# Optimization experiments

Measured on AMD Instinct MI355X. Metric: run time of the kernel, lower is better.

The kernel has to match this reference:

```python
import jax, jax.numpy as jnp
import numpy as np

DIM = 256
NEG_SLOPE = 0.01  # torch F.leaky_relu default


def setup_inputs() -> dict:
    key = jax.random.key(0)
    ks = jax.random.split(key, 10)
    B, O, I, D = 16, 64, 512, DIM
    q = jax.random.normal(ks[0], (B, O, D), dtype=jnp.float32)
    k = jax.random.normal(ks[1], (B, I, D), dtype=jnp.float32)
    v = jax.random.normal(ks[2], (B, I, D), dtype=jnp.float32)
    mask = jax.random.randint(ks[3], (B, I), 0, 2).astype(bool)  # 1/True = pad
    s = 1.0 / np.sqrt(2 * D)
    # score MLP: Linear(2D -> D), tanh, Linear(D -> 1)
    W1 = jax.random.normal(ks[4], (D, 2 * D), dtype=jnp.float32) * s
    b1 = jnp.zeros((D,), dtype=jnp.float32)
    W2 = jax.random.normal(ks[5], (1, D), dtype=jnp.float32) * (1.0 / np.sqrt(D))
    b2 = jnp.zeros((1,), dtype=jnp.float32)
    # output projection fw: Linear(D -> D)
    Wf = jax.random.normal(ks[6], (D, D), dtype=jnp.float32) * (1.0 / np.sqrt(D))
    bf = jnp.zeros((D,), dtype=jnp.float32)
    return {"q": q, "k": k, "v": v, "mask": mask,
            "W1": W1, "b1": b1, "W2": W2, "b2": b2, "Wf": Wf, "bf": bf}


def reference(q, k, v, mask, W1, b1, W2, b2, Wf, bf):
    # Linear over concat([q, k]) decomposes exactly: W1 @ [q;k] = W1q@q + W1k@k
    D = q.shape[-1]
    W1q, W1k = W1[:, :D], W1[:, D:]
    qp = jnp.einsum('bod,hd->boh', q, W1q)          # (B, O, D)
    kp = jnp.einsum('bid,hd->bih', k, W1k)          # (B, I, D)
    h = jnp.tanh(qp[:, :, None, :] + kp[:, None, :, :] + b1)  # (B, O, I, D)
    score = jnp.einsum('boih,h->boi', h, W2[0]) + b2[0]       # (B, O, I)
    score = jnp.where(mask[:, None, :], -jnp.inf, score)
    attn = jax.nn.softmax(score, axis=-1)           # (B, O, I)
    out = jnp.einsum('boi,bid->bod', attn, v)       # (B, O, D)
    out = out @ Wf.T + bf                           # dropout in eval mode = identity
    out = jnp.where(out >= 0, out, NEG_SLOPE * out) # leaky_relu
    return out, attn
```

## Files before the change

### kernel.cpp

```cpp
#include <hip/hip_runtime.h>
#include <math.h>

#define DIM 256
#define BATCH 16
#define NO 64
#define NI 512
#define NEG_SLOPE 0.01f
#define CSCALE 2.885390081777927f
#define OT 2

typedef float f32x4 __attribute__((ext_vector_type(4)));
typedef __bf16 bf16x8 __attribute__((ext_vector_type(8)));
typedef unsigned int u32x4 __attribute__((ext_vector_type(4)));

__device__ __forceinline__ void split2(float f, unsigned int& hi16, float& lo) {
  unsigned int u = __builtin_bit_cast(unsigned int, f);
  unsigned int h = (u + 0x7FFFu + ((u >> 16) & 1u)) & 0xFFFF0000u;
  hi16 = h >> 16;
  lo = f - __builtin_bit_cast(float, h);
}
__device__ __forceinline__ unsigned int rne16(float f) {
  unsigned int u = __builtin_bit_cast(unsigned int, f);
  return (u + 0x7FFFu + ((u >> 16) & 1u)) >> 16;
}

struct __align__(8) U2 { unsigned int x, y; };

#define OFF_AH 0
#define OFF_AL 9216
#define OFF_WH 18432
#define OFF_WL 27648

__global__ __launch_bounds__(256, 4) void proj_kernel(
    const float* __restrict__ q, const float* __restrict__ k,
    const float* __restrict__ W1, const float* __restrict__ b1,
    const float* __restrict__ Wf, const int* __restrict__ mask,
    float* __restrict__ Eq, float* __restrict__ Ek4, float* __restrict__ WfT)
{
  __shared__ __align__(16) char smemRaw[36864];
  __shared__ int idx_s[64];
  __shared__ int swtot[4];

  const int t  = threadIdx.x;
  const int bx = blockIdx.x;

  if (bx >= 576) {
    float* smem = (float*)smemRaw;
    const int tt = bx - 576;
    const int tr = tt >> 2, tc = tt & 3;
#pragma unroll
    for (int p = 0; p < 4; ++p) {
      int idx2 = p * 256 + t;
      int row = idx2 >> 4, j = idx2 & 15;
      float4 vv = *(const float4*)(Wf + (size_t)(tr * 64 + row) * 256 + tc * 64 + j * 4);
      *(float4*)&smem[row * 68 + j * 4] = vv;
    }
    __syncthreads();
#pragma unroll
    for (int p = 0; p < 4; ++p) {
      int idx2 = p * 256 + t;
      int row = idx2 >> 4, j = idx2 & 15;
      float4 ov;
      ov.x = smem[(j * 4 + 0) * 68 + row];
      ov.y = smem[(j * 4 + 1) * 68 + row];
      ov.z = smem[(j * 4 + 2) * 68 + row];
      ov.w = smem[(j * 4 + 3) * 68 + row];
      *(float4*)(WfT + (size_t)(tc * 64 + row) * 256 + tr * 64 + j * 4) = ov;
    }
    return;
  }

  const int mt = bx >> 2;
  const int nt = bx & 3;
  const int h0 = nt * 64;
  const bool isq = (mt < 16);

  const int srow = t >> 4;
  const int sc4  = t & 15;
  const int lane = t & 63, w = t >> 6;
  const int m0w = (w >> 1) * 32, n0w = (w & 1) * 32;
  const int lr = lane & 15, lg = lane >> 4;

  const float* src;
  int coff, bb = 0, jb0 = 0, cntb = 0;
  int rowg[4];

  if (isq) {
    src  = q + (size_t)(mt * 64) * DIM;
    coff = 0;
#pragma unroll
    for (int p = 0; p < 4; ++p) rowg[p] = srow + p * 16;
  } else {
    const int ki = mt - 16;
    bb  = ki >> 3;
    jb0 = (ki & 7) * 64;
    const int e0 = (mask[bb * NI + 2 * t] == 0);
    const int e1 = (mask[bb * NI + 2 * t + 1] == 0);
    const int ps = e0 + e1;
    int x = ps;
#pragma unroll
    for (int off = 1; off < 64; off <<= 1) {
      int y = __shfl_up(x, off, 64);
      if (lane >= off) x += y;
    }
    if (lane == 63) swtot[w] = x;
    if (t < 64) idx_s[t] = 0;
    __syncthreads();
    int woffv = 0;
#pragma unroll
    for (int w2 = 0; w2 < 4; ++w2) {
      int v_ = swtot[w2];
      if (w2 < w) woffv += v_;
      cntb += v_;
    }
    const int excl = woffv + x - ps;
    const int p0 = excl, p1 = excl + e0;
    if (e0 && p0 >= jb0 && p0 < jb0 + 64) idx_s[p0 - jb0] = 2 * t;
    if (e1 && p1 >= jb0 && p1 < jb0 + 64) idx_s[p1 - jb0] = 2 * t + 1;
    __syncthreads();
    if (jb0 >= cntb) return;
    src  = k + (size_t)bb * NI * DIM;
    coff = DIM;
#pragma unroll
    for (int p = 0; p < 4; ++p) rowg[p] = idx_s[srow + p * 16];
  }

  f32x4 acc[2][2] = {};

  float4 aR[4], wR[4];
#define LOADC(c0_)                                                              \
  _Pragma("unroll")                                                             \
  for (int p = 0; p < 4; ++p) {                                                 \
    aR[p] = *(const float4*)(src + (size_t)rowg[p] * DIM + (c0_) + sc4 * 4);    \
    wR[p] = *(const float4*)(W1 + (size_t)(h0 + srow + p * 16) * (2 * DIM) + coff + (c0_) + sc4 * 4); \
  }

  LOADC(0)

  for (int c = 0; c < 4; ++c) {
#pragma unroll
    for (int p = 0; p < 4; ++p) {
      int row = srow + p * 16;
      int boff = row * 144 + sc4 * 8;
      unsigned int h0_, h1_, h2_, h3_;
      float l0, l1, l2, l3;
      split2(aR[p].x, h0_, l0); split2(aR[p].y, h1_, l1);
      split2(aR[p].z, h2_, l2); split2(aR[p].w, h3_, l3);
      *(U2*)(smemRaw + OFF_AH + boff) = { h0_ | (h1_ << 16), h2_ | (h3_ << 16) };
      *(U2*)(smemRaw + OFF_AL + boff) = { rne16(l0) | (rne16(l1) << 16),
                                          rne16(l2) | (rne16(l3) << 16) };
      split2(wR[p].x, h0_, l0); split2(wR[p].y, h1_, l1);
      split2(wR[p].z, h2_, l2); split2(wR[p].w, h3_, l3);
      *(U2*)(smemRaw + OFF_WH + boff) = { h0_ | (h1_ << 16), h2_ | (h3_ << 16) };
      *(U2*)(smemRaw + OFF_WL + boff) = { rne16(l0) | (rne16(l1) << 16),
                                          rne16(l2) | (rne16(l3) << 16) };
    }
    __syncthreads();

    if (c < 3) { LOADC((c + 1) * 64) }

#pragma unroll
    for (int kk = 0; kk < 2; ++kk) {
      const int kb = kk * 64 + lg * 16;
      bf16x8 ah[2], al[2], bh[2], bl[2];
#pragma unroll
      for (int mi = 0; mi < 2; ++mi) {
        int row = m0w + mi * 16 + lr;
        ah[mi] = __builtin_bit_cast(bf16x8, *(const u32x4*)(smemRaw + OFF_AH + row * 144 + kb));
        al[mi] = __builtin_bit_cast(bf16x8, *(const u32x4*)(smemRaw + OFF_AL + row * 144 + kb));
      }
#pragma unroll
      for (int ni = 0; ni < 2; ++ni) {
        int row = n0w + ni * 16 + lr;
        bh[ni] = __builtin_bit_cast(bf16x8, *(const u32x4*)(smemRaw + OFF_WH + row * 144 + kb));
        bl[ni] = __builtin_bit_cast(bf16x8, *(const u32x4*)(smemRaw + OFF_WL + row * 144 + kb));
      }
#pragma unroll
      for (int mi = 0; mi < 2; ++mi)
#pragma unroll
        for (int ni = 0; ni < 2; ++ni) {
          acc[mi][ni] = __builtin_amdgcn_mfma_f32_16x16x32_bf16(ah[mi], bh[ni], acc[mi][ni], 0, 0, 0);
          acc[mi][ni] = __builtin_amdgcn_mfma_f32_16x16x32_bf16(ah[mi], bl[ni], acc[mi][ni], 0, 0, 0);
          acc[mi][ni] = __builtin_amdgcn_mfma_f32_16x16x32_bf16(al[mi], bh[ni], acc[mi][ni], 0, 0, 0);
        }
    }
    __syncthreads();
  }

  if (isq) {
    const int r0 = mt * 64;
#pragma unroll
    for (int ni = 0; ni < 2; ++ni) {
      int h = h0 + n0w + ni * 16 + lr;
      float b1v = b1[h];
#pragma unroll
      for (int mi = 0; mi < 2; ++mi)
#pragma unroll
        for (int rg = 0; rg < 4; ++rg) {
          int r = r0 + m0w + mi * 16 + lg * 4 + rg;
          Eq[(size_t)r * DIM + h] =
              __builtin_amdgcn_exp2f((acc[mi][ni][rg] + b1v) * CSCALE);
        }
    }
  } else {
    const int lim = cntb - jb0;
#pragma unroll
    for (int mi = 0; mi < 2; ++mi)
#pragma unroll
      for (int rg = 0; rg < 4; ++rg) {
        int local = m0w + mi * 16 + lg * 4 + rg;
        if (local < lim) {
          int pos = jb0 + local;
#pragma unroll
          for (int ni = 0; ni < 2; ++ni) {
            int h = h0 + n0w + ni * 16 + lr;
            Ek4[((size_t)(bb * 64 + (h >> 2)) * NI + pos) * 4 + (h & 3)] =
                __builtin_amdgcn_exp2f(acc[mi][ni][rg] * CSCALE);
          }
        }
      }
  }
}

__device__ __forceinline__ void f4arr(float4 v, float* a) {
  a[0] = v.x; a[1] = v.y; a[2] = v.z; a[3] = v.w;
}

__global__ __launch_bounds__(512, 4) void attn_kernel(
    const float* __restrict__ Eq, const float* __restrict__ Ek4,
    const float* __restrict__ v, const int* __restrict__ mask,
    const float* __restrict__ W2, const float* __restrict__ b2,
    const float* __restrict__ WfT, const float* __restrict__ bf,
    float* __restrict__ out, float* __restrict__ attn_out)
{
  __shared__ float sc[OT][NI];
  __shared__ int   idxs[NI];
  __shared__ float pvp[8][OT][DIM];
  __shared__ float o0[OT][DIM];
  __shared__ float red4[8][OT];
  __shared__ float redw[8];
  __shared__ int   swtot8[8];

  const int t    = threadIdx.x;
  const int lane = t & 63;
  const int wid  = t >> 6;

  const int blk  = blockIdx.x;
  const int tile = (blk & 7) * 64 + (blk >> 3);
  const int b    = tile >> 5;
  const int bo0  = b * 64 + (tile & 31) * OT;

  const int unm = (mask[b * NI + t] == 0) ? 1 : 0;
  unsigned long long bal = __ballot(unm);
  int my = __popcll(bal & ((1ull << lane) - 1ull));
  if (lane == 0) swtot8[wid] = __popcll(bal);

  float partial = (t < DIM) ? W2[t] : 0.f;
#pragma unroll
  for (int off = 32; off >= 1; off >>= 1) partial += __shfl_xor(partial, off, 64);
  if (lane == 0) redw[wid] = partial;
  __syncthreads();

  int cntb = 0, woffv = 0;
#pragma unroll
  for (int w = 0; w < 8; ++w) {
    int v_ = swtot8[w];
    if (w < wid) woffv += v_;
    cntb += v_;
  }
  const int myPos = unm ? (woffv + my) : -1;
  if (unm) idxs[myPos] = t;

  float sumw2 = 0.f;
#pragma unroll
  for (int w = 0; w < 8; ++w) sumw2 += redw[w];
  const float base = sumw2 + b2[0];

  const int j = t;
  const bool active = (j < cntb);
  const int jc = active ? j : (cntb > 0 ? cntb - 1 : 0);
  const float4* kb4 = (const float4*)Ek4 + (size_t)b * 64 * NI;
  const float* qrow0 = Eq + (size_t)(bo0 + 0) * DIM;
  const float* qrow1 = Eq + (size_t)(bo0 + 1) * DIM;

  float acc0 = 0.f, acc1 = 0.f;
  if (wid * 64 < cntb) {
#pragma unroll 8
    for (int hq = 0; hq < 64; ++hq) {
      float4 kq = kb4[(size_t)hq * NI + jc];
      float wr[4], q0r[4], q1r[4], kv[4];
      f4arr(*(const float4*)(W2 + hq * 4), wr);
      f4arr(*(const float4*)(qrow0 + hq * 4), q0r);
      f4arr(*(const float4*)(qrow1 + hq * 4), q1r);
      f4arr(kq, kv);
#pragma unroll
      for (int pr = 0; pr < 2; ++pr) {
        const int ea = pr * 2, eb = pr * 2 + 1;
        float A0 = fmaf(q0r[ea], kv[ea], 1.f);
        float B0 = fmaf(q0r[eb], kv[eb], 1.f);
        float N0 = fmaf(wr[eb], A0, wr[ea] * B0);
        acc0 = fmaf(N0, __builtin_amdgcn_rcpf(A0 * B0), acc0);
        float A1 = fmaf(q1r[ea], kv[ea], 1.f);
        float B1 = fmaf(q1r[eb], kv[eb], 1.f);
        float N1 = fmaf(wr[eb], A1, wr[ea] * B1);
        acc1 = fmaf(N1, __builtin_amdgcn_rcpf(A1 * B1), acc1);
      }
    }
  }

  float s0 = active ? (base - 2.f * acc0) : -INFINITY;
  float s1 = active ? (base - 2.f * acc1) : -INFINITY;

  float p0 = __builtin_amdgcn_exp2f(s0 * 1.4426950408889634f);
  float p1 = __builtin_amdgcn_exp2f(s1 * 1.4426950408889634f);
  float ps0 = p0, ps1 = p1;
#pragma unroll
  for (int off = 32; off >= 1; off >>= 1) {
    ps0 += __shfl_xor(ps0, off, 64);
    ps1 += __shfl_xor(ps1, off, 64);
  }
  __syncthreads();
  if (lane == 0) { red4[wid][0] = ps0; red4[wid][1] = ps1; }
  __syncthreads();
  float ss0 = 0.f, ss1 = 0.f;
#pragma unroll
  for (int w = 0; w < 8; ++w) { ss0 += red4[w][0]; ss1 += red4[w][1]; }
  const float a0 = p0 * __builtin_amdgcn_rcpf(ss0);
  const float a1 = p1 * __builtin_amdgcn_rcpf(ss1);
  sc[0][j] = a0;
  sc[1][j] = a1;
  __syncthreads();

  {
    float w0 = (myPos >= 0) ? sc[0][myPos] : 0.f;
    float w1 = (myPos >= 0) ? sc[1][myPos] : 0.f;
    attn_out[(size_t)(bo0 + 0) * NI + t] = w0;
    attn_out[(size_t)(bo0 + 1) * NI + t] = w1;
  }

  {
    const int d4 = lane;
    float4 av0 = {0.f, 0.f, 0.f, 0.f};
    float4 av1 = {0.f, 0.f, 0.f, 0.f};
    const float4* vb4 = (const float4*)(v + (size_t)b * NI * DIM);
    const int jend = min(wid * 64 + 64, cntb);
#pragma unroll 4
    for (int jb = wid * 64; jb < jend; ++jb) {
      int row = idxs[jb];
      float sa0 = sc[0][jb], sa1 = sc[1][jb];
      float4 vv = vb4[(size_t)row * 64 + d4];
      av0.x = fmaf(sa0, vv.x, av0.x);
      av0.y = fmaf(sa0, vv.y, av0.y);
      av0.z = fmaf(sa0, vv.z, av0.z);
      av0.w = fmaf(sa0, vv.w, av0.w);
      av1.x = fmaf(sa1, vv.x, av1.x);
      av1.y = fmaf(sa1, vv.y, av1.y);
      av1.z = fmaf(sa1, vv.z, av1.z);
      av1.w = fmaf(sa1, vv.w, av1.w);
    }
    *(float4*)&pvp[wid][0][d4 * 4] = av0;
    *(float4*)&pvp[wid][1][d4 * 4] = av1;
  }
  __syncthreads();
  {
    int oo = t >> 8, d = t & 255;
    float sacc = 0.f;
#pragma unroll
    for (int w = 0; w < 8; ++w) sacc += pvp[w][oo][d];
    o0[oo][d] = sacc;
  }
  __syncthreads();

  if (t < DIM) {
    const int d = t;
    float f0 = 0.f, f1 = 0.f;
#pragma unroll 8
    for (int e4 = 0; e4 < 64; ++e4) {
      float oa[4], ob[4];
      f4arr(*(const float4*)&o0[0][e4 * 4], oa);
      f4arr(*(const float4*)&o0[1][e4 * 4], ob);
#pragma unroll
      for (int c = 0; c < 4; ++c) {
        float wv = WfT[(size_t)(e4 * 4 + c) * DIM + d];
        f0 = fmaf(oa[c], wv, f0);
        f1 = fmaf(ob[c], wv, f1);
      }
    }
    float bfv = bf[d];
    f0 += bfv; f1 += bfv;
    f0 = (f0 >= 0.f) ? f0 : NEG_SLOPE * f0;
    f1 = (f1 >= 0.f) ? f1 : NEG_SLOPE * f1;
    out[(size_t)(bo0 + 0) * DIM + d] = f0;
    out[(size_t)(bo0 + 1) * DIM + d] = f1;
  }
}

extern "C" void kernel_launch(void* const* d_in, const int* in_sizes, int n_in,
                              void* d_out, int out_size, void* d_ws, size_t ws_size,
                              hipStream_t stream) {
  const float* q    = (const float*)d_in[0];
  const float* k    = (const float*)d_in[1];
  const float* v    = (const float*)d_in[2];
  const int*   mask = (const int*)d_in[3];
  const float* W1   = (const float*)d_in[4];
  const float* b1   = (const float*)d_in[5];
  const float* W2   = (const float*)d_in[6];
  const float* b2   = (const float*)d_in[7];
  const float* Wf   = (const float*)d_in[8];
  const float* bf   = (const float*)d_in[9];

  float* out      = (float*)d_out;
  float* attn_out = out + (size_t)BATCH * NO * DIM;

  float* Eq   = (float*)d_ws;
  float* Ek4  = Eq + (size_t)BATCH * NO * DIM;
  float* WfT  = Ek4 + (size_t)BATCH * DIM * NI;

  proj_kernel<<<592, 256, 0, stream>>>(q, k, W1, b1, Wf, mask, Eq, Ek4, WfT);
  attn_kernel<<<(BATCH * NO) / OT, 512, 0, stream>>>(Eq, Ek4, v, mask,
                                                     W2, b2, WfT, bf, out, attn_out);
}
```

Measured before the change: 121.6 us.

## Process four query rows per attention block and stage q rows in LDS

Raises the number of output rows per block from two to four, so each Ek4 and v load is reused across more queries. The block count halves and the tile mapping is adjusted to match. The query rows are now staged in shared memory instead of being read from global memory inside the hot loop. In exchange, register and LDS use per block grow, so launch bounds drop to 2 blocks per CU, and with fewer blocks occupancy and latency hiding may suffer.

```diff
diff --git a/kernel.cpp b/kernel.cpp
--- a/kernel.cpp
+++ b/kernel.cpp
@@ -7,7 +7,7 @@
 #define NI 512
 #define NEG_SLOPE 0.01f
 #define CSCALE 2.885390081777927f
-#define OT 2
+#define OT 4
 
 typedef float f32x4 __attribute__((ext_vector_type(4)));
 typedef __bf16 bf16x8 __attribute__((ext_vector_type(8)));
@@ -226,7 +226,7 @@
   a[0] = v.x; a[1] = v.y; a[2] = v.z; a[3] = v.w;
 }
 
-__global__ __launch_bounds__(512, 4) void attn_kernel(
+__global__ __launch_bounds__(512, 2) void attn_kernel(
     const float* __restrict__ Eq, const float* __restrict__ Ek4,
     const float* __restrict__ v, const int* __restrict__ mask,
     const float* __restrict__ W2, const float* __restrict__ b2,
@@ -235,6 +235,7 @@
 {
   __shared__ float sc[OT][NI];
   __shared__ int   idxs[NI];
+  __shared__ float qs[OT][DIM];
   __shared__ float pvp[8][OT][DIM];
   __shared__ float o0[OT][DIM];
   __shared__ float red4[8][OT];
@@ -246,15 +247,21 @@
   const int wid  = t >> 6;
 
   const int blk  = blockIdx.x;
-  const int tile = (blk & 7) * 64 + (blk >> 3);
-  const int b    = tile >> 5;
-  const int bo0  = b * 64 + (tile & 31) * OT;
+  const int tile = (blk & 7) * 32 + (blk >> 3);
+  const int b    = tile >> 4;
+  const int bo0  = b * 64 + (tile & 15) * OT;
 
   const int unm = (mask[b * NI + t] == 0) ? 1 : 0;
   unsigned long long bal = __ballot(unm);
   int my = __popcll(bal & ((1ull << lane) - 1ull));
   if (lane == 0) swtot8[wid] = __popcll(bal);
 
+  if (t < 256) {
+    const int r = t >> 6, part = t & 63;
+    *(float4*)&qs[r][part * 4] =
+        *(const float4*)(Eq + (size_t)(bo0 + r) * DIM + part * 4);
+  }
+
   float partial = (t < DIM) ? W2[t] : 0.f;
 #pragma unroll
   for (int off = 32; off >= 1; off >>= 1) partial += __shfl_xor(partial, off, 64);
@@ -280,118 +287,124 @@
   const bool active = (j < cntb);
   const int jc = active ? j : (cntb > 0 ? cntb - 1 : 0);
   const float4* kb4 = (const float4*)Ek4 + (size_t)b * 64 * NI;
-  const float* qrow0 = Eq + (size_t)(bo0 + 0) * DIM;
-  const float* qrow1 = Eq + (size_t)(bo0 + 1) * DIM;
-
-  float acc0 = 0.f, acc1 = 0.f;
+
+  float accv[OT] = {};
   if (wid * 64 < cntb) {
-#pragma unroll 8
+#pragma unroll 4
     for (int hq = 0; hq < 64; ++hq) {
       float4 kq = kb4[(size_t)hq * NI + jc];
-      float wr[4], q0r[4], q1r[4], kv[4];
+      float wr[4], kv[4];
       f4arr(*(const float4*)(W2 + hq * 4), wr);
-      f4arr(*(const float4*)(qrow0 + hq * 4), q0r);
-      f4arr(*(const float4*)(qrow1 + hq * 4), q1r);
       f4arr(kq, kv);
+      float qr[OT][4];
+#pragma unroll
+      for (int r = 0; r < OT; ++r) f4arr(*(const float4*)&qs[r][hq * 4], qr[r]);
 #pragma unroll
       for (int pr = 0; pr < 2; ++pr) {
         const int ea = pr * 2, eb = pr * 2 + 1;
-        float A0 = fmaf(q0r[ea], kv[ea], 1.f);
-        float B0 = fmaf(q0r[eb], kv[eb], 1.f);
-        float N0 = fmaf(wr[eb], A0, wr[ea] * B0);
-        acc0 = fmaf(N0, __builtin_amdgcn_rcpf(A0 * B0), acc0);
-        float A1 = fmaf(q1r[ea], kv[ea], 1.f);
-        float B1 = fmaf(q1r[eb], kv[eb], 1.f);
-        float N1 = fmaf(wr[eb], A1, wr[ea] * B1);
-        acc1 = fmaf(N1, __builtin_amdgcn_rcpf(A1 * B1), acc1);
-      }
-    }
-  }
-
-  float s0 = active ? (base - 2.f * acc0) : -INFINITY;
-  float s1 = active ? (base - 2.f * acc1) : -INFINITY;
-
-  float p0 = __builtin_amdgcn_exp2f(s0 * 1.4426950408889634f);
-  float p1 = __builtin_amdgcn_exp2f(s1 * 1.4426950408889634f);
-  float ps0 = p0, ps1 = p1;
-#pragma unroll
-  for (int off = 32; off >= 1; off >>= 1) {
-    ps0 += __shfl_xor(ps0, off, 64);
-    ps1 += __shfl_xor(ps1, off, 64);
-  }
-  __syncthreads();
-  if (lane == 0) { red4[wid][0] = ps0; red4[wid][1] = ps1; }
-  __syncthreads();
-  float ss0 = 0.f, ss1 = 0.f;
-#pragma unroll
-  for (int w = 0; w < 8; ++w) { ss0 += red4[w][0]; ss1 += red4[w][1]; }
-  const float a0 = p0 * __builtin_amdgcn_rcpf(ss0);
-  const float a1 = p1 * __builtin_amdgcn_rcpf(ss1);
-  sc[0][j] = a0;
-  sc[1][j] = a1;
-  __syncthreads();
-
-  {
-    float w0 = (myPos >= 0) ? sc[0][myPos] : 0.f;
-    float w1 = (myPos >= 0) ? sc[1][myPos] : 0.f;
-    attn_out[(size_t)(bo0 + 0) * NI + t] = w0;
-    attn_out[(size_t)(bo0 + 1) * NI + t] = w1;
+#pragma unroll
+        for (int r = 0; r < OT; ++r) {
+          float A = fmaf(qr[r][ea], kv[ea], 1.f);
+          float B = fmaf(qr[r][eb], kv[eb], 1.f);
+          float N = fmaf(wr[eb], A, wr[ea] * B);
+          accv[r] = fmaf(N, __builtin_amdgcn_rcpf(A * B), accv[r]);
+        }
+      }
+    }
+  }
+
+  float p[OT], psum[OT];
+#pragma unroll
+  for (int r = 0; r < OT; ++r) {
+    float s = active ? (base - 2.f * accv[r]) : -INFINITY;
+    p[r] = __builtin_amdgcn_exp2f(s * 1.4426950408889634f);
+    psum[r] = p[r];
+  }
+#pragma unroll
+  for (int off = 32; off >= 1; off >>= 1)
+#pragma unroll
+    for (int r = 0; r < OT; ++r) psum[r] += __shfl_xor(psum[r], off, 64);
+  __syncthreads();
+  if (lane == 0)
+#pragma unroll
+    for (int r = 0; r < OT; ++r) red4[wid][r] = psum[r];
+  __syncthreads();
+  float ss[OT] = {};
+#pragma unroll
+  for (int w = 0; w < 8; ++w)
+#pragma unroll
+    for (int r = 0; r < OT; ++r) ss[r] += red4[w][r];
+#pragma unroll
+  for (int r = 0; r < OT; ++r)
+    sc[r][j] = p[r] * __builtin_amdgcn_rcpf(ss[r]);
+  __syncthreads();
+
+#pragma unroll
+  for (int r = 0; r < OT; ++r) {
+    float wv = (myPos >= 0) ? sc[r][myPos] : 0.f;
+    attn_out[(size_t)(bo0 + r) * NI + t] = wv;
   }
 
   {
     const int d4 = lane;
-    float4 av0 = {0.f, 0.f, 0.f, 0.f};
-    float4 av1 = {0.f, 0.f, 0.f, 0.f};
+    float4 av[OT] = {};
     const float4* vb4 = (const float4*)(v + (size_t)b * NI * DIM);
     const int jend = min(wid * 64 + 64, cntb);
-#pragma unroll 4
+#pragma unroll 2
     for (int jb = wid * 64; jb < jend; ++jb) {
       int row = idxs[jb];
-      float sa0 = sc[0][jb], sa1 = sc[1][jb];
+      float sa[OT];
+#pragma unroll
+      for (int r = 0; r < OT; ++r) sa[r] = sc[r][jb];
       float4 vv = vb4[(size_t)row * 64 + d4];
-      av0.x = fmaf(sa0, vv.x, av0.x);
-      av0.y = fmaf(sa0, vv.y, av0.y);
-      av0.z = fmaf(sa0, vv.z, av0.z);
-      av0.w = fmaf(sa0, vv.w, av0.w);
-      av1.x = fmaf(sa1, vv.x, av1.x);
-      av1.y = fmaf(sa1, vv.y, av1.y);
-      av1.z = fmaf(sa1, vv.z, av1.z);
-      av1.w = fmaf(sa1, vv.w, av1.w);
-    }
-    *(float4*)&pvp[wid][0][d4 * 4] = av0;
-    *(float4*)&pvp[wid][1][d4 * 4] = av1;
+#pragma unroll
+      for (int r = 0; r < OT; ++r) {
+        av[r].x = fmaf(sa[r], vv.x, av[r].x);
+        av[r].y = fmaf(sa[r], vv.y, av[r].y);
+        av[r].z = fmaf(sa[r], vv.z, av[r].z);
+        av[r].w = fmaf(sa[r], vv.w, av[r].w);
+      }
+    }
+#pragma unroll
+    for (int r = 0; r < OT; ++r)
+      *(float4*)&pvp[wid][r][d4 * 4] = av[r];
   }
   __syncthreads();
   {
-    int oo = t >> 8, d = t & 255;
-    float sacc = 0.f;
-#pragma unroll
-    for (int w = 0; w < 8; ++w) sacc += pvp[w][oo][d];
-    o0[oo][d] = sacc;
+    const int ob = t >> 8, d = t & 255;
+#pragma unroll
+    for (int g = 0; g < 2; ++g) {
+      int oo = ob + g * 2;
+      float sacc = 0.f;
+#pragma unroll
+      for (int w = 0; w < 8; ++w) sacc += pvp[w][oo][d];
+      o0[oo][d] = sacc;
+    }
   }
   __syncthreads();
 
   if (t < DIM) {
     const int d = t;
-    float f0 = 0.f, f1 = 0.f;
+    float f[OT] = {};
 #pragma unroll 8
     for (int e4 = 0; e4 < 64; ++e4) {
-      float oa[4], ob[4];
-      f4arr(*(const float4*)&o0[0][e4 * 4], oa);
-      f4arr(*(const float4*)&o0[1][e4 * 4], ob);
+      float oa[OT][4];
+#pragma unroll
+      for (int r = 0; r < OT; ++r) f4arr(*(const float4*)&o0[r][e4 * 4], oa[r]);
 #pragma unroll
       for (int c = 0; c < 4; ++c) {
         float wv = WfT[(size_t)(e4 * 4 + c) * DIM + d];
-        f0 = fmaf(oa[c], wv, f0);
-        f1 = fmaf(ob[c], wv, f1);
+#pragma unroll
+        for (int r = 0; r < OT; ++r) f[r] = fmaf(oa[r][c], wv, f[r]);
       }
     }
     float bfv = bf[d];
-    f0 += bfv; f1 += bfv;
-    f0 = (f0 >= 0.f) ? f0 : NEG_SLOPE * f0;
-    f1 = (f1 >= 0.f) ? f1 : NEG_SLOPE * f1;
-    out[(size_t)(bo0 + 0) * DIM + d] = f0;
-    out[(size_t)(bo0 + 1) * DIM + d] = f1;
+#pragma unroll
+    for (int r = 0; r < OT; ++r) {
+      float fv = f[r] + bfv;
+      fv = (fv >= 0.f) ? fv : NEG_SLOPE * fv;
+      out[(size_t)(bo0 + r) * DIM + d] = fv;
+    }
   }
 }
 
```

New measurement: 131.1 us. 7.8% more time.

## Split score reduction across lane pairs, stage q/W2 in LDS, widen projection

Applied to the files above, without the earlier changes.

The score loop now gives two lanes to each unmasked key position, each summing half of the hidden dimension, and combines them with a shuffle. Positions are handled in two 256-wide passes of 32 per wave, so the compacted unmasked keys are spread over all waves instead of leaving trailing waves idle. The q rows and W2 are staged into shared memory, and the final Wf projection now uses all 512 threads, one output row per half-block. The occupancy hint in launch bounds is lowered from 4 to 2. This may allow more registers per thread but could reduce how many blocks run at once.

```diff
diff --git a/kernel.cpp b/kernel.cpp
--- a/kernel.cpp
+++ b/kernel.cpp
@@ -226,7 +226,7 @@
   a[0] = v.x; a[1] = v.y; a[2] = v.z; a[3] = v.w;
 }
 
-__global__ __launch_bounds__(512, 4) void attn_kernel(
+__global__ __launch_bounds__(512, 2) void attn_kernel(
     const float* __restrict__ Eq, const float* __restrict__ Ek4,
     const float* __restrict__ v, const int* __restrict__ mask,
     const float* __restrict__ W2, const float* __restrict__ b2,
@@ -235,9 +235,11 @@
 {
   __shared__ float sc[OT][NI];
   __shared__ int   idxs[NI];
+  __shared__ float qs[OT][DIM];
+  __shared__ float w2s[DIM];
   __shared__ float pvp[8][OT][DIM];
   __shared__ float o0[OT][DIM];
-  __shared__ float red4[8][OT];
+  __shared__ float red8[8][OT];
   __shared__ float redw[8];
   __shared__ int   swtot8[8];
 
@@ -255,6 +257,15 @@
   int my = __popcll(bal & ((1ull << lane) - 1ull));
   if (lane == 0) swtot8[wid] = __popcll(bal);
 
+  if (t < 128) {
+    const int r = t >> 6, part = t & 63;
+    *(float4*)&qs[r][part * 4] =
+        *(const float4*)(Eq + (size_t)(bo0 + r) * DIM + part * 4);
+  } else if (t < 192) {
+    const int part = t - 128;
+    *(float4*)&w2s[part * 4] = *(const float4*)(W2 + part * 4);
+  }
+
   float partial = (t < DIM) ? W2[t] : 0.f;
 #pragma unroll
   for (int off = 32; off >= 1; off >>= 1) partial += __shfl_xor(partial, off, 64);
@@ -276,59 +287,76 @@
   for (int w = 0; w < 8; ++w) sumw2 += redw[w];
   const float base = sumw2 + b2[0];
 
-  const int j = t;
-  const bool active = (j < cntb);
-  const int jc = active ? j : (cntb > 0 ? cntb - 1 : 0);
   const float4* kb4 = (const float4*)Ek4 + (size_t)b * 64 * NI;
-  const float* qrow0 = Eq + (size_t)(bo0 + 0) * DIM;
-  const float* qrow1 = Eq + (size_t)(bo0 + 1) * DIM;
-
-  float acc0 = 0.f, acc1 = 0.f;
-  if (wid * 64 < cntb) {
-#pragma unroll 8
-    for (int hq = 0; hq < 64; ++hq) {
-      float4 kq = kb4[(size_t)hq * NI + jc];
-      float wr[4], q0r[4], q1r[4], kv[4];
-      f4arr(*(const float4*)(W2 + hq * 4), wr);
-      f4arr(*(const float4*)(qrow0 + hq * 4), q0r);
-      f4arr(*(const float4*)(qrow1 + hq * 4), q1r);
-      f4arr(kq, kv);
-#pragma unroll
-      for (int pr = 0; pr < 2; ++pr) {
-        const int ea = pr * 2, eb = pr * 2 + 1;
-        float A0 = fmaf(q0r[ea], kv[ea], 1.f);
-        float B0 = fmaf(q0r[eb], kv[eb], 1.f);
-        float N0 = fmaf(wr[eb], A0, wr[ea] * B0);
-        acc0 = fmaf(N0, __builtin_amdgcn_rcpf(A0 * B0), acc0);
-        float A1 = fmaf(q1r[ea], kv[ea], 1.f);
-        float B1 = fmaf(q1r[eb], kv[eb], 1.f);
-        float N1 = fmaf(wr[eb], A1, wr[ea] * B1);
-        acc1 = fmaf(N1, __builtin_amdgcn_rcpf(A1 * B1), acc1);
+  const int half = lane & 1;
+  const int cpos = (wid << 5) + (lane >> 1);
+  const int hqb  = half << 5;
+  float psum[OT] = {};
+
+#pragma unroll
+  for (int pass = 0; pass < 2; ++pass) {
+    const int pb = pass << 8;
+    if (pb + (wid << 5) < cntb) {
+      const int jc0 = pb + cpos;
+      const bool act = jc0 < cntb;
+      const int jc = act ? jc0 : (cntb - 1);
+      float acc0 = 0.f, acc1 = 0.f;
+#pragma unroll 4
+      for (int hh = 0; hh < 32; ++hh) {
+        const int hq = hqb + hh;
+        float4 kq = kb4[(size_t)hq * NI + jc];
+        float wr[4], kv[4], q0r[4], q1r[4];
+        f4arr(*(const float4*)&w2s[hq * 4], wr);
+        f4arr(*(const float4*)&qs[0][hq * 4], q0r);
+        f4arr(*(const float4*)&qs[1][hq * 4], q1r);
+        f4arr(kq, kv);
+#pragma unroll
+        for (int pr = 0; pr < 2; ++pr) {
+          const int ea = pr * 2, eb = pr * 2 + 1;
+          float A0 = fmaf(q0r[ea], kv[ea], 1.f);
+          float B0 = fmaf(q0r[eb], kv[eb], 1.f);
+          float N0 = fmaf(wr[eb], A0, wr[ea] * B0);
+          acc0 = fmaf(N0, __builtin_amdgcn_rcpf(A0 * B0), acc0);
+          float A1 = fmaf(q1r[ea], kv[ea], 1.f);
+          float B1 = fmaf(q1r[eb], kv[eb], 1.f);
+          float N1 = fmaf(wr[eb], A1, wr[ea] * B1);
+          acc1 = fmaf(N1, __builtin_amdgcn_rcpf(A1 * B1), acc1);
+        }
       }
-    }
-  }
-
-  float s0 = active ? (base - 2.f * acc0) : -INFINITY;
-  float s1 = active ? (base - 2.f * acc1) : -INFINITY;
-
-  float p0 = __builtin_amdgcn_exp2f(s0 * 1.4426950408889634f);
-  float p1 = __builtin_amdgcn_exp2f(s1 * 1.4426950408889634f);
-  float ps0 = p0, ps1 = p1;
+      acc0 += __shfl_xor(acc0, 1, 64);
+      acc1 += __shfl_xor(acc1, 1, 64);
+      float s0 = act ? (base - 2.f * acc0) : -INFINITY;
+      float s1 = act ? (base - 2.f * acc1) : -INFINITY;
+      float p0 = __builtin_amdgcn_exp2f(s0 * 1.4426950408889634f);
+      float p1 = __builtin_amdgcn_exp2f(s1 * 1.4426950408889634f);
+      psum[0] += p0; psum[1] += p1;
+      sc[0][jc0] = p0;
+      sc[1][jc0] = p1;
+    }
+  }
+
 #pragma unroll
   for (int off = 32; off >= 1; off >>= 1) {
-    ps0 += __shfl_xor(ps0, off, 64);
-    ps1 += __shfl_xor(ps1, off, 64);
-  }
-  __syncthreads();
-  if (lane == 0) { red4[wid][0] = ps0; red4[wid][1] = ps1; }
+    psum[0] += __shfl_xor(psum[0], off, 64);
+    psum[1] += __shfl_xor(psum[1], off, 64);
+  }
+  if (lane == 0) { red8[wid][0] = psum[0]; red8[wid][1] = psum[1]; }
   __syncthreads();
   float ss0 = 0.f, ss1 = 0.f;
 #pragma unroll
-  for (int w = 0; w < 8; ++w) { ss0 += red4[w][0]; ss1 += red4[w][1]; }
-  const float a0 = p0 * __builtin_amdgcn_rcpf(ss0);
-  const float a1 = p1 * __builtin_amdgcn_rcpf(ss1);
-  sc[0][j] = a0;
-  sc[1][j] = a1;
+  for (int w = 0; w < 8; ++w) { ss0 += red8[w][0]; ss1 += red8[w][1]; }
+  const float inv0 = __builtin_amdgcn_rcpf(0.5f * ss0);
+  const float inv1 = __builtin_amdgcn_rcpf(0.5f * ss1);
+
+#pragma unroll
+  for (int pass = 0; pass < 2; ++pass) {
+    const int pb = pass << 8;
+    if (pb + (wid << 5) < cntb) {
+      const int jc0 = pb + cpos;
+      sc[0][jc0] *= inv0;
+      sc[1][jc0] *= inv1;
+    }
+  }
   __syncthreads();
 
   {
@@ -339,31 +367,34 @@
   }
 
   {
-    const int d4 = lane;
     float4 av0 = {0.f, 0.f, 0.f, 0.f};
     float4 av1 = {0.f, 0.f, 0.f, 0.f};
     const float4* vb4 = (const float4*)(v + (size_t)b * NI * DIM);
-    const int jend = min(wid * 64 + 64, cntb);
+#pragma unroll
+    for (int pass = 0; pass < 2; ++pass) {
+      const int start = (pass << 8) + (wid << 5);
+      const int jend = min(start + 32, cntb);
 #pragma unroll 4
-    for (int jb = wid * 64; jb < jend; ++jb) {
-      int row = idxs[jb];
-      float sa0 = sc[0][jb], sa1 = sc[1][jb];
-      float4 vv = vb4[(size_t)row * 64 + d4];
-      av0.x = fmaf(sa0, vv.x, av0.x);
-      av0.y = fmaf(sa0, vv.y, av0.y);
-      av0.z = fmaf(sa0, vv.z, av0.z);
-      av0.w = fmaf(sa0, vv.w, av0.w);
-      av1.x = fmaf(sa1, vv.x, av1.x);
-      av1.y = fmaf(sa1, vv.y, av1.y);
-      av1.z = fmaf(sa1, vv.z, av1.z);
-      av1.w = fmaf(sa1, vv.w, av1.w);
-    }
-    *(float4*)&pvp[wid][0][d4 * 4] = av0;
-    *(float4*)&pvp[wid][1][d4 * 4] = av1;
+      for (int jb = start; jb < jend; ++jb) {
+        int row = idxs[jb];
+        float sa0 = sc[0][jb], sa1 = sc[1][jb];
+        float4 vv = vb4[(size_t)row * 64 + lane];
+        av0.x = fmaf(sa0, vv.x, av0.x);
+        av0.y = fmaf(sa0, vv.y, av0.y);
+        av0.z = fmaf(sa0, vv.z, av0.z);
+        av0.w = fmaf(sa0, vv.w, av0.w);
+        av1.x = fmaf(sa1, vv.x, av1.x);
+        av1.y = fmaf(sa1, vv.y, av1.y);
+        av1.z = fmaf(sa1, vv.z, av1.z);
+        av1.w = fmaf(sa1, vv.w, av1.w);
+      }
+    }
+    *(float4*)&pvp[wid][0][lane * 4] = av0;
+    *(float4*)&pvp[wid][1][lane * 4] = av1;
   }
   __syncthreads();
   {
-    int oo = t >> 8, d = t & 255;
+    const int oo = t >> 8, d = t & 255;
     float sacc = 0.f;
 #pragma unroll
     for (int w = 0; w < 8; ++w) sacc += pvp[w][oo][d];
@@ -371,27 +402,20 @@
   }
   __syncthreads();
 
-  if (t < DIM) {
-    const int d = t;
-    float f0 = 0.f, f1 = 0.f;
+  {
+    const int oo = t >> 8, d = t & 255;
+    float f = 0.f;
 #pragma unroll 8
     for (int e4 = 0; e4 < 64; ++e4) {
-      float oa[4], ob[4];
-      f4arr(*(const float4*)&o0[0][e4 * 4], oa);
-      f4arr(*(const float4*)&o0[1][e4 * 4], ob);
-#pragma unroll
-      for (int c = 0; c < 4; ++c) {
-        float wv = WfT[(size_t)(e4 * 4 + c) * DIM + d];
-        f0 = fmaf(oa[c], wv, f0);
-        f1 = fmaf(ob[c], wv, f1);
-      }
-    }
-    float bfv = bf[d];
-    f0 += bfv; f1 += bfv;
-    f0 = (f0 >= 0.f) ? f0 : NEG_SLOPE * f0;
-    f1 = (f1 >= 0.f) ? f1 : NEG_SLOPE * f1;
-    out[(size_t)(bo0 + 0) * DIM + d] = f0;
-    out[(size_t)(bo0 + 1) * DIM + d] = f1;
+      float oa[4];
+      f4arr(*(const float4*)&o0[oo][e4 * 4], oa);
+#pragma unroll
+      for (int c = 0; c < 4; ++c)
+        f = fmaf(oa[c], WfT[(size_t)(e4 * 4 + c) * DIM + d], f);
+    }
+    f += bf[d];
+    f = (f >= 0.f) ? f : NEG_SLOPE * f;
+    out[(size_t)(bo0 + oo) * DIM + d] = f;
   }
 }
 
```

New measurement: 123.1 us. No clear change (+1.2%).
